# Kernel tuning notes

Measured on AMD Instinct MI355X. Metric: run time of the kernel, lower is better.

The kernel has to match this reference:

```python
import jax, jax.numpy as jnp
import numpy as np
from jax import lax

VDECAY, VTH, GRAD_WIN, GRAD_AMP = 0.5, 0.5, 0.5, 1.0

@jax.custom_vjp
def spike(v):
    return (v > VTH).astype(v.dtype)

def _spike_fwd(v):
    return spike(v), v

def _spike_bwd(v, g):
    # rectangular surrogate gradient
    win = (jnp.abs(v - VTH) <= GRAD_WIN).astype(g.dtype)
    return (GRAD_AMP * g * win,)

spike.defvjp(_spike_fwd, _spike_bwd)

def setup_inputs() -> dict:
    key = jax.random.key(0)
    ks = jax.random.split(key, 3)
    B, D_IN, T, H, D_OUT = 256, 700, 250, 1024, 20
    spike_data = (jax.random.uniform(ks[0], (B, D_IN, T)) < 0.1).astype(jnp.float32)
    W_hid = jax.random.normal(ks[1], (H, D_IN), dtype=jnp.float32) * (1.0 / np.sqrt(D_IN))
    W_out = jax.random.normal(ks[2], (D_OUT, H), dtype=jnp.float32) * (1.0 / np.sqrt(H))
    return {
        "spike_data": spike_data,
        "W_hid": W_hid,
        "W_out": W_out,
        "hid_spike0": jnp.zeros((B, H), jnp.float32),
        "hid_volt0": jnp.zeros((B, H), jnp.float32),
        "out_spike0": jnp.zeros((B, D_OUT), jnp.float32),
        "out_volt0": jnp.zeros((B, D_OUT), jnp.float32),
        "batch_size": 256,
        "spike_ts": 250,
    }

def reference(spike_data, W_hid, W_out, hid_spike0, hid_volt0, out_spike0, out_volt0, batch_size, spike_ts):
    # [B, D_in, T] -> [T, B, D_in] for scan over time
    xs = jnp.moveaxis(spike_data.reshape(batch_size, -1, spike_ts), -1, 0)

    def step(carry, s_in):
        hs, hv, os_, ov = carry
        hv = hv * VDECAY * (1.0 - hs) + s_in @ W_hid.T      # leaky integrate, reset on spike
        hs = spike(hv)                                       # hidden spikes
        ov = ov * VDECAY * (1.0 - os_) + hs @ W_out.T
        os_ = spike(ov)
        return (hs, hv, os_, ov), os_

    _, out_spikes = lax.scan(step, (hid_spike0, hid_volt0, out_spike0, out_volt0), xs)
    return jnp.sum(out_spikes, axis=0)  # [B, D_out] spike counts
```

## Files before the change

kernel.cpp:

```cpp
#include <hip/hip_runtime.h>
#include <stdint.h>

#define B      256
#define DIN    700
#define T      250
#define H      1024
#define DOUT   20
#define NW_IN  11
#define NW_INP 12
#define NW_H   16
#define LMAX   160
#define JSENT  44896

typedef unsigned long long u64;

__global__ void prep_weights(const float* __restrict__ W_hid,
                             const float* __restrict__ W_out,
                             float* __restrict__ Wt,
                             float* __restrict__ WoT) {
    int idx = blockIdx.x * 256 + threadIdx.x;
    if (blockIdx.x < 2800) {
        int d = idx / H;
        int h = idx - d * H;
        Wt[idx] = W_hid[h * DIN + d];
    } else {
        int i = idx - 2800 * 256;
        int h = i / DOUT;
        int o = i - h * DOUT;
        WoT[i] = W_out[o * H + h];
    }
}

__global__ void prep_bits(const float* __restrict__ spk,
                          u64* __restrict__ bits) {
    int b  = blockIdx.x >> 2;
    int wc = blockIdx.x & 3;
    int t  = threadIdx.x;
    if (t >= T) return;
    int w0 = wc * 3;
    int w1 = (wc == 3) ? NW_IN : w0 + 3;
    const float* base = spk + (size_t)b * DIN * T + t;
    for (int w = w0; w < w1; ++w) {
        u64 m = 0;
#pragma unroll
        for (int j = 0; j < 64; ++j) {
            int d = (w << 6) + j;
            if (d < DIN) {
                float x = base[(size_t)d * T];
                m |= (u64)(x > 0.5f) << j;
            }
        }
        bits[((size_t)b * T + t) * NW_INP + w] = m;
    }
}

__global__ void prep_lists(const u64* __restrict__ bits,
                           unsigned short* __restrict__ lists,
                           unsigned short* __restrict__ nrow) {
    int row = blockIdx.x * 256 + threadIdx.x;
    if (row >= B * T) return;
    const u64* wp = bits + (size_t)row * NW_INP;
    unsigned short* lp = lists + (size_t)row * LMAX;
    int pos = 0;
#pragma unroll
    for (int k = 0; k < 6; ++k) {
        u64 m = wp[k];
        if (k == 5) m &= (1ull << 30) - 1ull;
        while (m) {
            int bb = __builtin_ctzll(m);
            m &= m - 1;
            int j = (k << 6) + bb;
            if (pos < LMAX) lp[pos] = (unsigned short)(j * 128 + ((j & 7) << 4));
            ++pos;
        }
    }
    int cA = (pos + 7) >> 3;
    while (pos < cA * 8 && pos < LMAX) lp[pos++] = JSENT;
    int posB0 = pos;
#pragma unroll
    for (int k = 5; k < NW_IN; ++k) {
        u64 m = wp[k];
        if (k == 5) m &= ~((1ull << 30) - 1ull);
        while (m) {
            int bb = __builtin_ctzll(m);
            m &= m - 1;
            int jl = (k << 6) + bb - 350;
            if (pos < LMAX) lp[pos] = (unsigned short)(jl * 128 + ((jl & 7) << 4));
            ++pos;
        }
    }
    int cB = ((pos - posB0) + 7) >> 3;
    while (pos < LMAX) lp[pos++] = JSENT;
    nrow[row] = (unsigned short)(cA | (cB << 8));
}

__global__ void __launch_bounds__(512, 2)
hidden_slice2(const unsigned short* __restrict__ lists,
              const unsigned short* __restrict__ nrow,
              const float* __restrict__ Wt,
              const float* __restrict__ hs0,
              const float* __restrict__ hv0,
              u64* __restrict__ hsbits) {
    __shared__ float wlds[351 * 32];
    __shared__ float cur[250 * 32];

    int s    = blockIdx.x;
    int b    = blockIdx.y;
    int tid  = threadIdx.x;
    int wv   = tid >> 6;
    int lane = tid & 63;
    int g    = lane >> 3;
    int li   = lane & 7;
    int lxor = li << 4;

    for (int p = 0; p < 2; ++p) {
        {
            int jr  = tid >> 3;
            int lis = tid & 7;
#pragma unroll
            for (int base_j = 0; base_j < 384; base_j += 64) {
                int j = base_j + jr;
                if (j < 351) {
                    float4 v;
                    if (j < 350)
                        v = *(const float4*)(Wt + (size_t)(p * 350 + j) * H + s * 32 + lis * 4);
                    else
                        v = make_float4(0.0f, 0.0f, 0.0f, 0.0f);
                    *(float4*)((char*)wlds + j * 128 + ((lis ^ (j & 7)) << 4)) = v;
                }
            }
        }
        __syncthreads();

        for (int sweep = 0; sweep < 4; ++sweep) {
            int r = sweep * 64 + wv * 8 + g;
            if (r < 250) {
                int row = b * T + r;
                unsigned cc = nrow[row];
                int cA = cc & 0xff;
                int c  = p ? ((cc >> 8) & 0xff) : cA;
                const uint4* qp = (const uint4*)(lists + (size_t)row * LMAX + (p ? cA * 8 : 0));

                float a0, a1, a2, a3;
                if (p == 0) {
                    a0 = a1 = a2 = a3 = 0.0f;
                } else {
                    float4 cv = *(const float4*)((char*)cur + r * 128 + lxor);
                    a0 = cv.x; a1 = cv.y; a2 = cv.z; a3 = cv.w;
                }

                if (c > 0) {
                    uint4 w4 = qp[0];
                    int ch = 0;
                    for (;;) {
                        uint4 nw = (ch + 1 < c) ? qp[ch + 1] : w4;
                        int e0 = w4.x & 0xffff, e1 = w4.x >> 16;
                        int e2 = w4.y & 0xffff, e3 = w4.y >> 16;
                        int e4 = w4.z & 0xffff, e5 = w4.z >> 16;
                        int e6 = w4.w & 0xffff, e7 = w4.w >> 16;
                        float4 v0 = *(const float4*)((char*)wlds + (e0 ^ lxor));
                        float4 v1 = *(const float4*)((char*)wlds + (e1 ^ lxor));
                        float4 v2 = *(const float4*)((char*)wlds + (e2 ^ lxor));
                        float4 v3 = *(const float4*)((char*)wlds + (e3 ^ lxor));
                        float4 v4 = *(const float4*)((char*)wlds + (e4 ^ lxor));
                        float4 v5 = *(const float4*)((char*)wlds + (e5 ^ lxor));
                        float4 v6 = *(const float4*)((char*)wlds + (e6 ^ lxor));
                        float4 v7 = *(const float4*)((char*)wlds + (e7 ^ lxor));
                        a0 += v0.x; a1 += v0.y; a2 += v0.z; a3 += v0.w;
                        a0 += v1.x; a1 += v1.y; a2 += v1.z; a3 += v1.w;
                        a0 += v2.x; a1 += v2.y; a2 += v2.z; a3 += v2.w;
                        a0 += v3.x; a1 += v3.y; a2 += v3.z; a3 += v3.w;
                        a0 += v4.x; a1 += v4.y; a2 += v4.z; a3 += v4.w;
                        a0 += v5.x; a1 += v5.y; a2 += v5.z; a3 += v5.w;
                        a0 += v6.x; a1 += v6.y; a2 += v6.z; a3 += v6.w;
                        a0 += v7.x; a1 += v7.y; a2 += v7.z; a3 += v7.w;
                        ++ch;
                        if (ch >= c) break;
                        w4 = nw;
                    }
                }
                float4 o; o.x = a0; o.y = a1; o.z = a2; o.w = a3;
                *(float4*)((char*)cur + r * 128 + lxor) = o;
            }
        }
        __syncthreads();
    }

    if (wv == 0) {
        int l = lane & 31;
        int h = s * 32 + l;
        float keep = hv0[b * H + h] * 0.5f * (1.0f - hs0[b * H + h]);
        unsigned* hp = (unsigned*)hsbits;
        float c = cur[l];
        for (int t = 0; t < T; ++t) {
            float cn = (t + 1 < T) ? cur[(t + 1) * 32 + l] : 0.0f;
            float hv = keep + c;
            bool sp = hv > 0.5f;
            keep = sp ? 0.0f : hv * 0.5f;
            u64 ball = __ballot(sp);
            if (lane == 0)
                hp[(size_t)(b * T + t) * 32 + s] = (unsigned)ball;
            c = cn;
        }
    }
}

__global__ void __launch_bounds__(1024)
hidden_fused(const u64* __restrict__ bits,
             const float* __restrict__ Wt,
             const float* __restrict__ hs0,
             const float* __restrict__ hv0,
             u64* __restrict__ hsbits) {
    __shared__ int idx_l[2][256];

    int b = blockIdx.x;
    int h = threadIdx.x;
    int wv   = h >> 6;
    int lane = h & 63;

    float keep = hv0[b * H + h] * 0.5f * (1.0f - hs0[b * H + h]);

    const u64* bb = bits + (size_t)b * T * NW_INP;

    for (int t = 0; t < T; ++t) {
        const u64* wp = bb + (size_t)t * NW_INP;
        u64 w[NW_IN];
#pragma unroll
        for (int k = 0; k < NW_IN; ++k) w[k] = wp[k];

        int base[NW_IN + 1];
        base[0] = 0;
#pragma unroll
        for (int k = 0; k < NW_IN; ++k) base[k + 1] = base[k] + __popcll(w[k]);
        int n = base[NW_IN];

        int buf = t & 1;
        if (wv < NW_IN) {
            u64 m = w[wv];
            if ((m >> lane) & 1ull) {
                int pos = base[wv] + __popcll(m & ((1ull << lane) - 1ull));
                idx_l[buf][pos] = (wv << 6) + lane;
            }
        }
        __syncthreads();

        const int* il = idx_l[buf];
        float cur2 = 0.0f;
        int i = 0;
        for (; i + 8 <= n; i += 8) {
            int j0 = il[i + 0], j1 = il[i + 1], j2 = il[i + 2], j3 = il[i + 3];
            int j4 = il[i + 4], j5 = il[i + 5], j6 = il[i + 6], j7 = il[i + 7];
            float v0 = Wt[(size_t)j0 * H + h];
            float v1 = Wt[(size_t)j1 * H + h];
            float v2 = Wt[(size_t)j2 * H + h];
            float v3 = Wt[(size_t)j3 * H + h];
            float v4 = Wt[(size_t)j4 * H + h];
            float v5 = Wt[(size_t)j5 * H + h];
            float v6 = Wt[(size_t)j6 * H + h];
            float v7 = Wt[(size_t)j7 * H + h];
            cur2 += v0; cur2 += v1; cur2 += v2; cur2 += v3;
            cur2 += v4; cur2 += v5; cur2 += v6; cur2 += v7;
        }
        for (; i < n; ++i) cur2 += Wt[(size_t)il[i] * H + h];

        float hv = keep + cur2;
        bool sp = hv > 0.5f;
        keep = sp ? 0.0f : hv * 0.5f;
        u64 ball = __ballot(sp);
        if (lane == 0)
            hsbits[((size_t)b * T + t) * NW_H + wv] = ball;
    }
}

__global__ void __launch_bounds__(256)
out_currents(const u64* __restrict__ hsbits,
             const float* __restrict__ WoT,
             float* __restrict__ Iout) {
    __shared__ int lidx[4][2][256];

    int wv   = threadIdx.x >> 6;
    int lane = threadIdx.x & 63;
    int row  = blockIdx.x * 4 + wv;

    const u64* wp = hsbits + (size_t)row * NW_H;

    float acc = 0.0f;
#pragma unroll
    for (int g = 0; g < 4; ++g) {
        u64 w[4];
#pragma unroll
        for (int k = 0; k < 4; ++k) w[k] = wp[g * 4 + k];

        int base[5];
        base[0] = 0;
#pragma unroll
        for (int k = 0; k < 4; ++k) base[k + 1] = base[k] + __popcll(w[k]);
        int n = base[4];

        int buf = g & 1;
#pragma unroll
        for (int k = 0; k < 4; ++k) {
            u64 m = w[k];
            if ((m >> lane) & 1ull) {
                int pos = base[k] + __popcll(m & ((1ull << lane) - 1ull));
                lidx[wv][buf][pos] = ((g * 4 + k) << 6) + lane;
            }
        }
        __syncthreads();

        const int* il = lidx[wv][buf];
        int i = 0;
        for (; i + 4 <= n; i += 4) {
            int j0 = il[i + 0], j1 = il[i + 1], j2 = il[i + 2], j3 = il[i + 3];
            if (lane < DOUT) {
                float v0 = WoT[(size_t)j0 * DOUT + lane];
                float v1 = WoT[(size_t)j1 * DOUT + lane];
                float v2 = WoT[(size_t)j2 * DOUT + lane];
                float v3 = WoT[(size_t)j3 * DOUT + lane];
                acc += v0; acc += v1; acc += v2; acc += v3;
            }
        }
        for (; i < n; ++i) {
            if (lane < DOUT) acc += WoT[(size_t)il[i] * DOUT + lane];
        }
    }
    if (lane < DOUT) Iout[(size_t)row * DOUT + lane] = acc;
}

__global__ void __launch_bounds__(256)
out_scan(const float* __restrict__ Iout,
         const float* __restrict__ os0,
         const float* __restrict__ ov0,
         float* __restrict__ outp) {
    __shared__ float pan[T * DOUT];

    int b   = blockIdx.x;
    int tid = threadIdx.x;

    const float* src = Iout + (size_t)b * T * DOUT;
#pragma unroll
    for (int k = 0; k < 20; ++k) {
        int i = k * 256 + tid;
        if (i < T * DOUT) pan[i] = src[i];
    }
    __syncthreads();

    if (tid < DOUT) {
        int o = tid;
        int idx = b * DOUT + o;
        float ov = ov0[idx];
        float os = os0[idx];
        float keep = ov * 0.5f * (1.0f - os);
        float cnt = 0.0f;
#pragma unroll 5
        for (int t = 0; t < T; ++t) {
            float v = keep + pan[t * DOUT + o];
            float sp = (v > 0.5f) ? 1.0f : 0.0f;
            cnt += sp;
            keep = v * 0.5f * (1.0f - sp);
        }
        outp[idx] = cnt;
    }
}

extern "C" void kernel_launch(void* const* d_in, const int* in_sizes, int n_in,
                              void* d_out, int out_size, void* d_ws, size_t ws_size,
                              hipStream_t stream) {
    const float* spike = (const float*)d_in[0];
    const float* W_hid = (const float*)d_in[1];
    const float* W_out = (const float*)d_in[2];
    const float* hs0   = (const float*)d_in[3];
    const float* hv0   = (const float*)d_in[4];
    const float* os0   = (const float*)d_in[5];
    const float* ov0   = (const float*)d_in[6];
    float* outp = (float*)d_out;

    char* ws = (char*)d_ws;
    float*          Wt     = (float*)(ws);
    float*          WoT    = (float*)(ws + 2867200);
    u64*            bits   = (u64*)  (ws + 2949120);
    u64*            hsbits = (u64*)  (ws + 9093120);
    float*          Iout   = (float*)(ws + 17285120);
    unsigned short* lists  = (unsigned short*)(ws + 22405120);
    unsigned short* nrow   = (unsigned short*)(ws + 42885120);
    const size_t need = 43013120;

    prep_weights<<<2880, 256, 0, stream>>>(W_hid, W_out, Wt, WoT);
    prep_bits<<<1024, 256, 0, stream>>>(spike, bits);

    if (ws_size >= need) {
        prep_lists<<<250, 256, 0, stream>>>(bits, lists, nrow);
        hidden_slice2<<<dim3(32, 256), 512, 0, stream>>>(lists, nrow, Wt, hs0, hv0, hsbits);
    } else {
        hidden_fused<<<B, 1024, 0, stream>>>(bits, Wt, hs0, hv0, hsbits);
    }

    out_currents<<<16000, 256, 0, stream>>>(hsbits, WoT, Iout);
    out_scan<<<B, 256, 0, stream>>>(Iout, os0, ov0, outp);
}
```

Before: 1.016 ms.

## Parallelize sparse list build per wave and sort rows by chunk count

The spike-index list build now gives each row to one wavefront, using ballot-style popcount prefix sums in LDS instead of a serial ctz loop per thread. This is meant to remove the long serial tail in prep_lists, which launched only 250 blocks. A new sort_rows kernel does a counting sort of the timesteps in each batch by chunk count, so the 8-lane groups within a wave in hidden_slice2 process rows of similar length and diverge less. The cost is an extra kernel launch and one permutation load per row.

```diff
diff --git a/kernel.cpp b/kernel.cpp
--- a/kernel.cpp
+++ b/kernel.cpp
@@ -54,49 +54,97 @@
     }
 }
 
-__global__ void prep_lists(const u64* __restrict__ bits,
-                           unsigned short* __restrict__ lists,
-                           unsigned short* __restrict__ nrow) {
-    int row = blockIdx.x * 256 + threadIdx.x;
-    if (row >= B * T) return;
+__global__ void __launch_bounds__(256)
+prep_lists2(const u64* __restrict__ bits,
+            unsigned short* __restrict__ lists,
+            unsigned short* __restrict__ nrow) {
+    __shared__ unsigned short scr[4][LMAX];
+
+    int wv   = threadIdx.x >> 6;
+    int lane = threadIdx.x & 63;
+    int row  = blockIdx.x * 4 + wv;
+
     const u64* wp = bits + (size_t)row * NW_INP;
-    unsigned short* lp = lists + (size_t)row * LMAX;
-    int pos = 0;
+    u64 mw = (lane < NW_IN) ? wp[lane] : 0ull;
+
+    for (int i = lane; i < LMAX; i += 64) scr[wv][i] = (unsigned short)JSENT;
+
+    u64 lowmask = (1ull << lane) - 1ull;
+
+    int baseA = 0;
 #pragma unroll
     for (int k = 0; k < 6; ++k) {
-        u64 m = wp[k];
+        u64 m = __shfl(mw, k);
         if (k == 5) m &= (1ull << 30) - 1ull;
-        while (m) {
-            int bb = __builtin_ctzll(m);
-            m &= m - 1;
-            int j = (k << 6) + bb;
-            if (pos < LMAX) lp[pos] = (unsigned short)(j * 128 + ((j & 7) << 4));
-            ++pos;
-        }
-    }
-    int cA = (pos + 7) >> 3;
-    while (pos < cA * 8 && pos < LMAX) lp[pos++] = JSENT;
-    int posB0 = pos;
+        if ((m >> lane) & 1ull) {
+            int pos = baseA + __popcll(m & lowmask);
+            int j = (k << 6) + lane;
+            if (pos < LMAX)
+                scr[wv][pos] = (unsigned short)(j * 128 + ((j & 7) << 4));
+        }
+        baseA += __popcll(m);
+    }
+    int cA = (baseA + 7) >> 3;
+    int bs = cA * 8;
+
+    int baseB = 0;
 #pragma unroll
     for (int k = 5; k < NW_IN; ++k) {
-        u64 m = wp[k];
+        u64 m = __shfl(mw, k);
         if (k == 5) m &= ~((1ull << 30) - 1ull);
-        while (m) {
-            int bb = __builtin_ctzll(m);
-            m &= m - 1;
-            int jl = (k << 6) + bb - 350;
-            if (pos < LMAX) lp[pos] = (unsigned short)(jl * 128 + ((jl & 7) << 4));
-            ++pos;
-        }
-    }
-    int cB = ((pos - posB0) + 7) >> 3;
-    while (pos < LMAX) lp[pos++] = JSENT;
-    nrow[row] = (unsigned short)(cA | (cB << 8));
+        if ((m >> lane) & 1ull) {
+            int pos = bs + baseB + __popcll(m & lowmask);
+            int jl = (k << 6) + lane - 350;
+            if (pos < LMAX)
+                scr[wv][pos] = (unsigned short)(jl * 128 + ((jl & 7) << 4));
+        }
+        baseB += __popcll(m);
+    }
+    int cB = (baseB + 7) >> 3;
+
+    if (lane == 0) nrow[row] = (unsigned short)(cA | (cB << 8));
+
+    __syncthreads();
+
+    const unsigned* s32 = (const unsigned*)scr[wv];
+    unsigned* g32 = (unsigned*)(lists + (size_t)row * LMAX);
+    g32[lane] = s32[lane];
+    if (lane < 16) g32[64 + lane] = s32[64 + lane];
+}
+
+__global__ void __launch_bounds__(256)
+sort_rows(const unsigned short* __restrict__ nrow,
+          unsigned char* __restrict__ permA,
+          unsigned char* __restrict__ permB) {
+    __shared__ unsigned cntA[24], cntB[24], offA[24], offB[24];
+    int b = blockIdx.x, tid = threadIdx.x;
+    if (tid < 24) { cntA[tid] = 0; cntB[tid] = 0; }
+    __syncthreads();
+    int cA = 0, cB = 0;
+    if (tid < T) {
+        unsigned cc = nrow[b * T + tid];
+        cA = cc & 0xff;          if (cA > 23) cA = 23;
+        cB = (cc >> 8) & 0xff;   if (cB > 23) cB = 23;
+        atomicAdd(&cntA[cA], 1);
+        atomicAdd(&cntB[cB], 1);
+    }
+    __syncthreads();
+    if (tid == 0) { unsigned s = 0; for (int i = 0; i < 24; ++i) { offA[i] = s; s += cntA[i]; cntA[i] = 0; } }
+    if (tid == 1) { unsigned s = 0; for (int i = 0; i < 24; ++i) { offB[i] = s; s += cntB[i]; cntB[i] = 0; } }
+    __syncthreads();
+    if (tid < T) {
+        unsigned pA = offA[cA] + atomicAdd(&cntA[cA], 1);
+        unsigned pB = offB[cB] + atomicAdd(&cntB[cB], 1);
+        permA[b * 256 + pA] = (unsigned char)tid;
+        permB[b * 256 + pB] = (unsigned char)tid;
+    }
 }
 
 __global__ void __launch_bounds__(512, 2)
 hidden_slice2(const unsigned short* __restrict__ lists,
               const unsigned short* __restrict__ nrow,
+              const unsigned char* __restrict__ permA,
+              const unsigned char* __restrict__ permB,
               const float* __restrict__ Wt,
               const float* __restrict__ hs0,
               const float* __restrict__ hv0,
@@ -132,9 +180,12 @@
         }
         __syncthreads();
 
+        const unsigned char* pm = (p ? permB : permA) + b * 256;
+
         for (int sweep = 0; sweep < 4; ++sweep) {
-            int r = sweep * 64 + wv * 8 + g;
-            if (r < 250) {
+            int rr = sweep * 64 + wv * 8 + g;
+            if (rr < 250) {
+                int r   = pm[rr];
                 int row = b * T + r;
                 unsigned cc = nrow[row];
                 int cA = cc & 0xff;
@@ -383,14 +434,17 @@
     float*          Iout   = (float*)(ws + 17285120);
     unsigned short* lists  = (unsigned short*)(ws + 22405120);
     unsigned short* nrow   = (unsigned short*)(ws + 42885120);
-    const size_t need = 43013120;
+    unsigned char*  permA  = (unsigned char*)(ws + 43013120);
+    unsigned char*  permB  = (unsigned char*)(ws + 43078656);
+    const size_t need = 43144192;
 
     prep_weights<<<2880, 256, 0, stream>>>(W_hid, W_out, Wt, WoT);
     prep_bits<<<1024, 256, 0, stream>>>(spike, bits);
 
     if (ws_size >= need) {
-        prep_lists<<<250, 256, 0, stream>>>(bits, lists, nrow);
-        hidden_slice2<<<dim3(32, 256), 512, 0, stream>>>(lists, nrow, Wt, hs0, hv0, hsbits);
+        prep_lists2<<<16000, 256, 0, stream>>>(bits, lists, nrow);
+        sort_rows<<<B, 256, 0, stream>>>(nrow, permA, permB);
+        hidden_slice2<<<dim3(32, 256), 512, 0, stream>>>(lists, nrow, permA, permB, Wt, hs0, hv0, hsbits);
     } else {
         hidden_fused<<<B, 1024, 0, stream>>>(bits, Wt, hs0, hv0, hsbits);
     }
```

After: 994.8 us. -2.1%, faster.
